# Kernel tuning notes

Measured on AMD Instinct MI355X. Metric: run time of the kernel, lower is better.

## Reference

```python
import jax, jax.numpy as jnp
import numpy as np

N = 102400          # total nodes across the batched session graphs
D = 256             # item_dim == output_dim (so fc_out is None)
NUM_SEGMENTS = 2048 # number of graphs in the batch
TAO = 1.0


def setup_inputs() -> dict:
    key = jax.random.key(0)
    k0, k1, k2, k3, k4 = jax.random.split(key, 5)
    ifeat = jax.random.normal(k0, (N, D), dtype=jnp.float32)
    seg_ids = jnp.sort(jax.random.randint(k1, (N,), 0, NUM_SEGMENTS, dtype=jnp.int32))
    scale = 1.0 / np.sqrt(D)
    Wu = jax.random.normal(k2, (D, D), dtype=jnp.float32) * scale  # fc_u weight (no bias)
    Wv = jax.random.normal(k3, (D, D), dtype=jnp.float32) * scale  # fc_v weight
    bv = jnp.zeros((D,), dtype=jnp.float32)                        # fc_v bias
    we = jax.random.normal(k4, (D,), dtype=jnp.float32) * scale    # fc_e weight [1, D] -> [D]
    return {"ifeat": ifeat, "Wu": Wu, "Wv": Wv, "bv": bv, "we": we, "seg_ids": seg_ids}


def reference(ifeat, Wu, Wv, bv, we, seg_ids):
    # --- anchor: per-graph mean of ifeat (pooling_type == 'imean') ---
    counts = jax.ops.segment_sum(jnp.ones((ifeat.shape[0],), ifeat.dtype), seg_ids,
                                 num_segments=NUM_SEGMENTS)            # [B]
    anchor = jax.ops.segment_sum(ifeat, seg_ids, num_segments=NUM_SEGMENTS)
    anchor = anchor / jnp.maximum(counts, 1.0)[:, None]                # [B, D]

    # --- attention scores: e = fc_e(sigmoid(fc_u(ifeat) + broadcast(fc_v(anchor)))) ---
    ifeat_u = ifeat @ Wu.T                                             # [N, D]
    feat_v = anchor @ Wv.T + bv                                        # [B, D]
    e = jax.nn.sigmoid(ifeat_u + feat_v[seg_ids]) @ we                 # [N]
    logits = e / TAO

    # --- segment softmax over ragged per-graph node groups ---
    m = jax.ops.segment_max(logits, seg_ids, num_segments=NUM_SEGMENTS)  # [B]
    z = jnp.exp(logits - m[seg_ids])                                     # [N]
    denom = jax.ops.segment_sum(z, seg_ids, num_segments=NUM_SEGMENTS)   # [B]
    alpha = z / denom[seg_ids]                                           # [N]

    # --- attention-weighted segment sum (fc_out is None since item_dim == output_dim) ---
    rst = jax.ops.segment_sum(ifeat * alpha[:, None], seg_ids,
                              num_segments=NUM_SEGMENTS)               # [B, D]
    return jnp.concatenate([rst, anchor], axis=1)                       # [B, 2D]
```

## Files before the change

### kernel.cpp

```cpp
#include <hip/hip_runtime.h>
#include <math.h>

#define NN 102400
#define D 256
#define B 2048

typedef __bf16 bf16x8 __attribute__((ext_vector_type(8)));
typedef float f32x4 __attribute__((ext_vector_type(4)));

__global__ __launch_bounds__(256)
void k_anchor3(const float* __restrict__ ifeat, const int* __restrict__ seg,
               float* __restrict__ out, float* __restrict__ anc_buf,
               int* __restrict__ seg_start) {
    __shared__ int sb[2];
    __shared__ float red[4][256];
    int b = blockIdx.x;
    int t = threadIdx.x;
    if (t < 2) {
        int target = b + t;
        int lo = 0, hi = NN;
        while (lo < hi) { int mid = (lo + hi) >> 1; if (seg[mid] < target) lo = mid + 1; else hi = mid; }
        sb[t] = lo;
        if (t == 0) seg_start[b] = lo;
        if (t == 1 && b == B - 1) seg_start[B] = lo;
    }
    __syncthreads();
    int w = t >> 6, l = t & 63;
    int s = sb[0], e = sb[1];
    const float* bp = ifeat + (size_t)l * 4;
    float4 a0 = make_float4(0.f, 0.f, 0.f, 0.f), a1 = a0, a2 = a0, a3 = a0, a4 = a0, a5 = a0;
    int i = s + w;
    for (; i + 20 < e; i += 24) {
        float4 v0 = *(const float4*)(bp + (size_t)(i +  0) * D);
        float4 v1 = *(const float4*)(bp + (size_t)(i +  4) * D);
        float4 v2 = *(const float4*)(bp + (size_t)(i +  8) * D);
        float4 v3 = *(const float4*)(bp + (size_t)(i + 12) * D);
        float4 v4 = *(const float4*)(bp + (size_t)(i + 16) * D);
        float4 v5 = *(const float4*)(bp + (size_t)(i + 20) * D);
        a0.x += v0.x; a0.y += v0.y; a0.z += v0.z; a0.w += v0.w;
        a1.x += v1.x; a1.y += v1.y; a1.z += v1.z; a1.w += v1.w;
        a2.x += v2.x; a2.y += v2.y; a2.z += v2.z; a2.w += v2.w;
        a3.x += v3.x; a3.y += v3.y; a3.z += v3.z; a3.w += v3.w;
        a4.x += v4.x; a4.y += v4.y; a4.z += v4.z; a4.w += v4.w;
        a5.x += v5.x; a5.y += v5.y; a5.z += v5.z; a5.w += v5.w;
    }
    for (; i < e; i += 4) {
        float4 v = *(const float4*)(bp + (size_t)i * D);
        a0.x += v.x; a0.y += v.y; a0.z += v.z; a0.w += v.w;
    }
    float4 acc = make_float4(((a0.x + a1.x) + (a2.x + a3.x)) + (a4.x + a5.x),
                             ((a0.y + a1.y) + (a2.y + a3.y)) + (a4.y + a5.y),
                             ((a0.z + a1.z) + (a2.z + a3.z)) + (a4.z + a5.z),
                             ((a0.w + a1.w) + (a2.w + a3.w)) + (a4.w + a5.w));
    *(float4*)&red[w][l * 4] = acc;
    __syncthreads();
    float sum = (red[0][t] + red[1][t]) + (red[2][t] + red[3][t]);
    int cnt = e - s;
    float inv = 1.0f / (float)(cnt > 0 ? cnt : 1);
    float v = sum * inv;
    out[(size_t)b * 512 + 256 + t] = v;
    anc_buf[(size_t)b * D + t] = v;
}

__global__ __launch_bounds__(256)
void k_featv3(const float* __restrict__ anc_buf, const float* __restrict__ Wv,
              const float* __restrict__ bv, float* __restrict__ feat_v) {
    __shared__ __bf16 As[16][264];
    int b0 = blockIdx.x * 16;
    int t = threadIdx.x;
    int lane = t & 63, w = t >> 6;
    int ln15 = lane & 15, lg = lane >> 4;
#pragma unroll
    for (int r = 0; r < 16; ++r) As[r][t] = (__bf16)anc_buf[(size_t)(b0 + r) * D + t];
    __syncthreads();
    bf16x8 afr[8];
#pragma unroll
    for (int kc = 0; kc < 8; ++kc) afr[kc] = *(const bf16x8*)&As[ln15][kc * 32 + lg * 8];
#pragma unroll
    for (int q = 0; q < 4; ++q) {
        int jt = w * 4 + q;
        f32x4 acc = (f32x4){0.f, 0.f, 0.f, 0.f};
#pragma unroll
        for (int kc = 0; kc < 8; ++kc) {
            const float* wp = Wv + (size_t)(jt * 16 + ln15) * D + kc * 32 + lg * 8;
            float4 p = *(const float4*)(wp);
            float4 r4 = *(const float4*)(wp + 4);
            bf16x8 bfr;
            bfr[0] = (__bf16)p.x;  bfr[1] = (__bf16)p.y;  bfr[2] = (__bf16)p.z;  bfr[3] = (__bf16)p.w;
            bfr[4] = (__bf16)r4.x; bfr[5] = (__bf16)r4.y; bfr[6] = (__bf16)r4.z; bfr[7] = (__bf16)r4.w;
            acc = __builtin_amdgcn_mfma_f32_16x16x32_bf16(afr[kc], bfr, acc, 0, 0, 0);
        }
        float bvj = bv[jt * 16 + ln15];
#pragma unroll
        for (int r = 0; r < 4; ++r) {
            feat_v[(size_t)(b0 + lg * 4 + r) * D + jt * 16 + ln15] = acc[r] + bvj;
        }
    }
}

__global__ __launch_bounds__(1024, 4)
void k_attn_e_mfma(const float* __restrict__ ifeat, const float* __restrict__ Wu,
                   const float* __restrict__ feat_v, const float* __restrict__ we,
                   const int* __restrict__ seg_ids, float* __restrict__ e_out) {
    __shared__ __bf16 Bs[256 * 256];

    int tx = threadIdx.x;
    int lane = tx & 63;
    int w = tx >> 6;
    int ln15 = lane & 15;
    int lg = lane >> 4;

    {
        int jl = tx >> 2, kh = tx & 3;
        const float* wp = Wu + (size_t)jl * D + kh * 64;
        char* rowp = (char*)Bs + jl * 512;
        int sw = (jl & 7) << 4;
#pragma unroll
        for (int q = 0; q < 8; ++q) {
            float4 b0 = *(const float4*)(wp + q * 8);
            float4 b1 = *(const float4*)(wp + q * 8 + 4);
            bf16x8 v;
            v[0] = (__bf16)b0.x; v[1] = (__bf16)b0.y; v[2] = (__bf16)b0.z; v[3] = (__bf16)b0.w;
            v[4] = (__bf16)b1.x; v[5] = (__bf16)b1.y; v[6] = (__bf16)b1.z; v[7] = (__bf16)b1.w;
            *(bf16x8*)(rowp + ((kh * 128 + q * 16) ^ sw)) = v;
        }
    }
    __syncthreads();

    int swr = (ln15 & 7) << 4;
    int klo = lg * 16;
    const char* bbase = (const char*)Bs + ln15 * 512;
    const float* feph = feat_v + ln15;
    const float* weh  = we + ln15;

    int wgid = blockIdx.x * 16 + w;

    for (int item = wgid; item < NN / 16; item += 4096) {
        int nb = item * 16;
        const float* ap = ifeat + (size_t)(nb + ln15) * D + lg * 8;

        f32x4 a0 = (f32x4){0.f,0.f,0.f,0.f}, a1 = a0, a2 = a0, a3 = a0,
              a4 = a0, a5 = a0, a6 = a0, a7 = a0,
              a8 = a0, a9 = a0, a10 = a0, a11 = a0,
              a12 = a0, a13 = a0, a14 = a0, a15 = a0;

        float4 xc = *(const float4*)(ap);
        float4 yc = *(const float4*)(ap + 4);
        float4 x1 = *(const float4*)(ap + 32);
        float4 y1 = *(const float4*)(ap + 36);
#pragma unroll 1
        for (int ch = 0; ch < 8; ++ch) {
            int nx = ((ch + 2) & 7) * 32;
            float4 x2 = *(const float4*)(ap + nx);
            float4 y2 = *(const float4*)(ap + nx + 4);
            bf16x8 af;
            af[0] = (__bf16)xc.x; af[1] = (__bf16)xc.y; af[2] = (__bf16)xc.z; af[3] = (__bf16)xc.w;
            af[4] = (__bf16)yc.x; af[5] = (__bf16)yc.y; af[6] = (__bf16)yc.z; af[7] = (__bf16)yc.w;
            int kb = (ch * 64 + klo) ^ swr;
            a0  = __builtin_amdgcn_mfma_f32_16x16x32_bf16(af, *(const bf16x8*)(bbase +  0 * 8192 + kb), a0,  0, 0, 0);
            a1  = __builtin_amdgcn_mfma_f32_16x16x32_bf16(af, *(const bf16x8*)(bbase +  1 * 8192 + kb), a1,  0, 0, 0);
            a2  = __builtin_amdgcn_mfma_f32_16x16x32_bf16(af, *(const bf16x8*)(bbase +  2 * 8192 + kb), a2,  0, 0, 0);
            a3  = __builtin_amdgcn_mfma_f32_16x16x32_bf16(af, *(const bf16x8*)(bbase +  3 * 8192 + kb), a3,  0, 0, 0);
            a4  = __builtin_amdgcn_mfma_f32_16x16x32_bf16(af, *(const bf16x8*)(bbase +  4 * 8192 + kb), a4,  0, 0, 0);
            a5  = __builtin_amdgcn_mfma_f32_16x16x32_bf16(af, *(const bf16x8*)(bbase +  5 * 8192 + kb), a5,  0, 0, 0);
            a6  = __builtin_amdgcn_mfma_f32_16x16x32_bf16(af, *(const bf16x8*)(bbase +  6 * 8192 + kb), a6,  0, 0, 0);
            a7  = __builtin_amdgcn_mfma_f32_16x16x32_bf16(af, *(const bf16x8*)(bbase +  7 * 8192 + kb), a7,  0, 0, 0);
            a8  = __builtin_amdgcn_mfma_f32_16x16x32_bf16(af, *(const bf16x8*)(bbase +  8 * 8192 + kb), a8,  0, 0, 0);
            a9  = __builtin_amdgcn_mfma_f32_16x16x32_bf16(af, *(const bf16x8*)(bbase +  9 * 8192 + kb), a9,  0, 0, 0);
            a10 = __builtin_amdgcn_mfma_f32_16x16x32_bf16(af, *(const bf16x8*)(bbase + 10 * 8192 + kb), a10, 0, 0, 0);
            a11 = __builtin_amdgcn_mfma_f32_16x16x32_bf16(af, *(const bf16x8*)(bbase + 11 * 8192 + kb), a11, 0, 0, 0);
            a12 = __builtin_amdgcn_mfma_f32_16x16x32_bf16(af, *(const bf16x8*)(bbase + 12 * 8192 + kb), a12, 0, 0, 0);
            a13 = __builtin_amdgcn_mfma_f32_16x16x32_bf16(af, *(const bf16x8*)(bbase + 13 * 8192 + kb), a13, 0, 0, 0);
            a14 = __builtin_amdgcn_mfma_f32_16x16x32_bf16(af, *(const bf16x8*)(bbase + 14 * 8192 + kb), a14, 0, 0, 0);
            a15 = __builtin_amdgcn_mfma_f32_16x16x32_bf16(af, *(const bf16x8*)(bbase + 15 * 8192 + kb), a15, 0, 0, 0);
            xc = x1; yc = y1; x1 = x2; y1 = y2;
        }

        int r0 = nb + lg * 4;
        const float* fp0 = feph + (size_t)seg_ids[r0 + 0] * D;
        const float* fp1 = feph + (size_t)seg_ids[r0 + 1] * D;
        const float* fp2 = feph + (size_t)seg_ids[r0 + 2] * D;
        const float* fp3 = feph + (size_t)seg_ids[r0 + 3] * D;
        float part0 = 0.f, part1 = 0.f, part2 = 0.f, part3 = 0.f;

#define EPI(AC, CT) { \
    float w_ = weh[(CT) * 16]; \
    part0 += w_ * __builtin_amdgcn_rcpf(1.f + __expf(-(AC[0] + fp0[(CT) * 16]))); \
    part1 += w_ * __builtin_amdgcn_rcpf(1.f + __expf(-(AC[1] + fp1[(CT) * 16]))); \
    part2 += w_ * __builtin_amdgcn_rcpf(1.f + __expf(-(AC[2] + fp2[(CT) * 16]))); \
    part3 += w_ * __builtin_amdgcn_rcpf(1.f + __expf(-(AC[3] + fp3[(CT) * 16]))); }

        EPI(a0, 0)  EPI(a1, 1)  EPI(a2, 2)  EPI(a3, 3)
        EPI(a4, 4)  EPI(a5, 5)  EPI(a6, 6)  EPI(a7, 7)
        EPI(a8, 8)  EPI(a9, 9)  EPI(a10, 10) EPI(a11, 11)
        EPI(a12, 12) EPI(a13, 13) EPI(a14, 14) EPI(a15, 15)
#undef EPI

#pragma unroll
        for (int off = 8; off >= 1; off >>= 1) {
            part0 += __shfl_xor(part0, off, 64);
            part1 += __shfl_xor(part1, off, 64);
            part2 += __shfl_xor(part2, off, 64);
            part3 += __shfl_xor(part3, off, 64);
        }
        if (ln15 == 0) {
            float4 o = make_float4(part0, part1, part2, part3);
            *(float4*)&e_out[r0] = o;
        }
    }
}

__global__ void k_softmax_rst(const float* __restrict__ ifeat, const int* __restrict__ seg_start,
                              const float* __restrict__ e, float* __restrict__ out) {
    int b = blockIdx.x;
    int t = threadIdx.x;
    int w = t >> 6, l = t & 63;
    int s = seg_start[b], en = seg_start[b + 1];
    float m = -1e30f;
    for (int i = s + t; i < en; i += 256) m = fmaxf(m, e[i]);
#pragma unroll
    for (int off = 32; off >= 1; off >>= 1) m = fmaxf(m, __shfl_xor(m, off, 64));
    __shared__ float red[4];
    if ((t & 63) == 0) red[t >> 6] = m;
    __syncthreads();
    float mall = fmaxf(fmaxf(red[0], red[1]), fmaxf(red[2], red[3]));
    float dsum = 0.f;
    for (int i = s + t; i < en; i += 256) dsum += __expf(e[i] - mall);
#pragma unroll
    for (int off = 32; off >= 1; off >>= 1) dsum += __shfl_xor(dsum, off, 64);
    __shared__ float red2[4];
    if ((t & 63) == 0) red2[t >> 6] = dsum;
    __syncthreads();
    float denom = red2[0] + red2[1] + red2[2] + red2[3];
    float invd = (en > s) ? 1.0f / denom : 0.f;

    const float* bp = ifeat + (size_t)l * 4;
    float4 c0 = make_float4(0.f, 0.f, 0.f, 0.f), c1 = c0, c2 = c0, c3 = c0, c4 = c0, c5 = c0;
    int i = s + w;
    for (; i + 20 < en; i += 24) {
        float al0 = __expf(e[i +  0] - mall) * invd;
        float al1 = __expf(e[i +  4] - mall) * invd;
        float al2 = __expf(e[i +  8] - mall) * invd;
        float al3 = __expf(e[i + 12] - mall) * invd;
        float al4 = __expf(e[i + 16] - mall) * invd;
        float al5 = __expf(e[i + 20] - mall) * invd;
        float4 v0 = *(const float4*)(bp + (size_t)(i +  0) * D);
        float4 v1 = *(const float4*)(bp + (size_t)(i +  4) * D);
        float4 v2 = *(const float4*)(bp + (size_t)(i +  8) * D);
        float4 v3 = *(const float4*)(bp + (size_t)(i + 12) * D);
        float4 v4 = *(const float4*)(bp + (size_t)(i + 16) * D);
        float4 v5 = *(const float4*)(bp + (size_t)(i + 20) * D);
        c0.x += v0.x * al0; c0.y += v0.y * al0; c0.z += v0.z * al0; c0.w += v0.w * al0;
        c1.x += v1.x * al1; c1.y += v1.y * al1; c1.z += v1.z * al1; c1.w += v1.w * al1;
        c2.x += v2.x * al2; c2.y += v2.y * al2; c2.z += v2.z * al2; c2.w += v2.w * al2;
        c3.x += v3.x * al3; c3.y += v3.y * al3; c3.z += v3.z * al3; c3.w += v3.w * al3;
        c4.x += v4.x * al4; c4.y += v4.y * al4; c4.z += v4.z * al4; c4.w += v4.w * al4;
        c5.x += v5.x * al5; c5.y += v5.y * al5; c5.z += v5.z * al5; c5.w += v5.w * al5;
    }
    for (; i < en; i += 4) {
        float al = __expf(e[i] - mall) * invd;
        float4 v = *(const float4*)(bp + (size_t)i * D);
        c0.x += v.x * al; c0.y += v.y * al; c0.z += v.z * al; c0.w += v.w * al;
    }
    float4 acc = make_float4(((c0.x + c1.x) + (c2.x + c3.x)) + (c4.x + c5.x),
                             ((c0.y + c1.y) + (c2.y + c3.y)) + (c4.y + c5.y),
                             ((c0.z + c1.z) + (c2.z + c3.z)) + (c4.z + c5.z),
                             ((c0.w + c1.w) + (c2.w + c3.w)) + (c4.w + c5.w));
    __shared__ float red3[4][256];
    *(float4*)&red3[w][l * 4] = acc;
    __syncthreads();
    out[(size_t)b * 512 + t] = (red3[0][t] + red3[1][t]) + (red3[2][t] + red3[3][t]);
}

extern "C" void kernel_launch(void* const* d_in, const int* in_sizes, int n_in,
                              void* d_out, int out_size, void* d_ws, size_t ws_size,
                              hipStream_t stream) {
    const float* ifeat = (const float*)d_in[0];
    const float* Wu    = (const float*)d_in[1];
    const float* Wv    = (const float*)d_in[2];
    const float* bv    = (const float*)d_in[3];
    const float* we    = (const float*)d_in[4];
    const int*   seg   = (const int*)d_in[5];
    float* out = (float*)d_out;

    char* ws = (char*)d_ws;
    int*   seg_start = (int*)ws;
    float* feat_v    = (float*)(ws + 16384);
    float* e_buf     = (float*)(ws + 16384 + (size_t)B * D * 4);
    float* anc_buf   = (float*)(ws + 16384 + (size_t)B * D * 4 + 512 * 1024);

    k_anchor3<<<B, 256, 0, stream>>>(ifeat, seg, out, anc_buf, seg_start);
    k_featv3<<<B / 16, 256, 0, stream>>>(anc_buf, Wv, bv, feat_v);
    k_attn_e_mfma<<<256, 1024, 0, stream>>>(ifeat, Wu, feat_v, we, seg, e_buf);
    k_softmax_rst<<<B, 256, 0, stream>>>(ifeat, seg_start, e_buf, out);
}
```

Measured before the change: 108.0 us.

## Transpose feat_v layout for vectorized prefetch and halve attention block size

The feat_v output of k_featv3 is stored in a transposed per-row layout, so each lane's 16 epilogue values become contiguous and can be loaded as four float4s. These loads are issued before the MFMA loop, letting the gather latency overlap with compute instead of stalling the epilogue. The attention kernel also drops from 1024 to 512 threads per block with launch bounds of one block per CU, so each wave handles twice as many tiles. The extra float4 prefetch registers raise register pressure, and the lower wave count reduces latency hiding.

```diff
diff --git a/kernel.cpp b/kernel.cpp
--- a/kernel.cpp
+++ b/kernel.cpp
@@ -64,7 +64,7 @@
 
 __global__ __launch_bounds__(256)
 void k_featv3(const float* __restrict__ anc_buf, const float* __restrict__ Wv,
-              const float* __restrict__ bv, float* __restrict__ feat_v) {
+              const float* __restrict__ bv, float* __restrict__ fvT) {
     __shared__ __bf16 As[16][264];
     int b0 = blockIdx.x * 16;
     int t = threadIdx.x;
@@ -93,14 +93,14 @@
         float bvj = bv[jt * 16 + ln15];
 #pragma unroll
         for (int r = 0; r < 4; ++r) {
-            feat_v[(size_t)(b0 + lg * 4 + r) * D + jt * 16 + ln15] = acc[r] + bvj;
-        }
-    }
-}
-
-__global__ __launch_bounds__(1024, 4)
+            fvT[(size_t)(b0 + lg * 4 + r) * 256 + ln15 * 16 + jt] = acc[r] + bvj;
+        }
+    }
+}
+
+__global__ __launch_bounds__(512, 1)
 void k_attn_e_mfma(const float* __restrict__ ifeat, const float* __restrict__ Wu,
-                   const float* __restrict__ feat_v, const float* __restrict__ we,
+                   const float* __restrict__ fvT, const float* __restrict__ we,
                    const int* __restrict__ seg_ids, float* __restrict__ e_out) {
     __shared__ __bf16 Bs[256 * 256];
 
@@ -111,18 +111,18 @@
     int lg = lane >> 4;
 
     {
-        int jl = tx >> 2, kh = tx & 3;
-        const float* wp = Wu + (size_t)jl * D + kh * 64;
+        int jl = tx >> 1, kh = tx & 1;
+        const float* wp = Wu + (size_t)jl * D + kh * 128;
         char* rowp = (char*)Bs + jl * 512;
         int sw = (jl & 7) << 4;
 #pragma unroll
-        for (int q = 0; q < 8; ++q) {
+        for (int q = 0; q < 16; ++q) {
             float4 b0 = *(const float4*)(wp + q * 8);
             float4 b1 = *(const float4*)(wp + q * 8 + 4);
             bf16x8 v;
             v[0] = (__bf16)b0.x; v[1] = (__bf16)b0.y; v[2] = (__bf16)b0.z; v[3] = (__bf16)b0.w;
             v[4] = (__bf16)b1.x; v[5] = (__bf16)b1.y; v[6] = (__bf16)b1.z; v[7] = (__bf16)b1.w;
-            *(bf16x8*)(rowp + ((kh * 128 + q * 16) ^ sw)) = v;
+            *(bf16x8*)(rowp + ((kh * 256 + q * 16) ^ sw)) = v;
         }
     }
     __syncthreads();
@@ -130,13 +130,27 @@
     int swr = (ln15 & 7) << 4;
     int klo = lg * 16;
     const char* bbase = (const char*)Bs + ln15 * 512;
-    const float* feph = feat_v + ln15;
     const float* weh  = we + ln15;
 
-    int wgid = blockIdx.x * 16 + w;
-
-    for (int item = wgid; item < NN / 16; item += 4096) {
+    int wgid = blockIdx.x * 8 + w;
+
+    for (int item = wgid; item < NN / 16; item += 2048) {
         int nb = item * 16;
+        int r0 = nb + lg * 4;
+
+        const float* q0 = fvT + (size_t)seg_ids[r0 + 0] * 256 + ln15 * 16;
+        const float* q1 = fvT + (size_t)seg_ids[r0 + 1] * 256 + ln15 * 16;
+        const float* q2 = fvT + (size_t)seg_ids[r0 + 2] * 256 + ln15 * 16;
+        const float* q3 = fvT + (size_t)seg_ids[r0 + 3] * 256 + ln15 * 16;
+        float4 fvA0 = *(const float4*)(q0 +  0), fvA1 = *(const float4*)(q0 +  4),
+               fvA2 = *(const float4*)(q0 +  8), fvA3 = *(const float4*)(q0 + 12);
+        float4 fvB0 = *(const float4*)(q1 +  0), fvB1 = *(const float4*)(q1 +  4),
+               fvB2 = *(const float4*)(q1 +  8), fvB3 = *(const float4*)(q1 + 12);
+        float4 fvC0 = *(const float4*)(q2 +  0), fvC1 = *(const float4*)(q2 +  4),
+               fvC2 = *(const float4*)(q2 +  8), fvC3 = *(const float4*)(q2 + 12);
+        float4 fvD0 = *(const float4*)(q3 +  0), fvD1 = *(const float4*)(q3 +  4),
+               fvD2 = *(const float4*)(q3 +  8), fvD3 = *(const float4*)(q3 + 12);
+
         const float* ap = ifeat + (size_t)(nb + ln15) * D + lg * 8;
 
         f32x4 a0 = (f32x4){0.f,0.f,0.f,0.f}, a1 = a0, a2 = a0, a3 = a0,
@@ -176,24 +190,19 @@
             xc = x1; yc = y1; x1 = x2; y1 = y2;
         }
 
-        int r0 = nb + lg * 4;
-        const float* fp0 = feph + (size_t)seg_ids[r0 + 0] * D;
-        const float* fp1 = feph + (size_t)seg_ids[r0 + 1] * D;
-        const float* fp2 = feph + (size_t)seg_ids[r0 + 2] * D;
-        const float* fp3 = feph + (size_t)seg_ids[r0 + 3] * D;
         float part0 = 0.f, part1 = 0.f, part2 = 0.f, part3 = 0.f;
 
-#define EPI(AC, CT) { \
+#define EPI(AC, CT, FQ, FC) { \
     float w_ = weh[(CT) * 16]; \
-    part0 += w_ * __builtin_amdgcn_rcpf(1.f + __expf(-(AC[0] + fp0[(CT) * 16]))); \
-    part1 += w_ * __builtin_amdgcn_rcpf(1.f + __expf(-(AC[1] + fp1[(CT) * 16]))); \
-    part2 += w_ * __builtin_amdgcn_rcpf(1.f + __expf(-(AC[2] + fp2[(CT) * 16]))); \
-    part3 += w_ * __builtin_amdgcn_rcpf(1.f + __expf(-(AC[3] + fp3[(CT) * 16]))); }
-
-        EPI(a0, 0)  EPI(a1, 1)  EPI(a2, 2)  EPI(a3, 3)
-        EPI(a4, 4)  EPI(a5, 5)  EPI(a6, 6)  EPI(a7, 7)
-        EPI(a8, 8)  EPI(a9, 9)  EPI(a10, 10) EPI(a11, 11)
-        EPI(a12, 12) EPI(a13, 13) EPI(a14, 14) EPI(a15, 15)
+    part0 += w_ * __builtin_amdgcn_rcpf(1.f + __expf(-(AC[0] + fvA##FQ.FC))); \
+    part1 += w_ * __builtin_amdgcn_rcpf(1.f + __expf(-(AC[1] + fvB##FQ.FC))); \
+    part2 += w_ * __builtin_amdgcn_rcpf(1.f + __expf(-(AC[2] + fvC##FQ.FC))); \
+    part3 += w_ * __builtin_amdgcn_rcpf(1.f + __expf(-(AC[3] + fvD##FQ.FC))); }
+
+        EPI(a0,  0, 0, x) EPI(a1,  1, 0, y) EPI(a2,  2, 0, z) EPI(a3,  3, 0, w)
+        EPI(a4,  4, 1, x) EPI(a5,  5, 1, y) EPI(a6,  6, 1, z) EPI(a7,  7, 1, w)
+        EPI(a8,  8, 2, x) EPI(a9,  9, 2, y) EPI(a10, 10, 2, z) EPI(a11, 11, 2, w)
+        EPI(a12, 12, 3, x) EPI(a13, 13, 3, y) EPI(a14, 14, 3, z) EPI(a15, 15, 3, w)
 #undef EPI
 
 #pragma unroll
@@ -291,6 +300,6 @@
 
     k_anchor3<<<B, 256, 0, stream>>>(ifeat, seg, out, anc_buf, seg_start);
     k_featv3<<<B / 16, 256, 0, stream>>>(anc_buf, Wv, bv, feat_v);
-    k_attn_e_mfma<<<256, 1024, 0, stream>>>(ifeat, Wu, feat_v, we, seg, e_buf);
+    k_attn_e_mfma<<<256, 512, 0, stream>>>(ifeat, Wu, feat_v, we, seg, e_buf);
     k_softmax_rst<<<B, 256, 0, stream>>>(ifeat, seg_start, e_buf, out);
 }
```

Result: faster. 101.0 us (-6.5%).
